# Kernel tuning notes

Measured on AMD Instinct MI355X. Metric: run time of the kernel, lower is better.

Reference implementation:

```python
import jax, jax.numpy as jnp
import numpy as np

V, D, NH, T_MAX, L, MLP = 50257, 1024, 16, 1024, 12, 4
HD = D // NH
F = D * MLP
B, T = 2, 1024


def setup_inputs() -> dict:
    key = jax.random.key(0)
    ks = jax.random.split(key, 16)
    s = 0.02
    inp = {
        'tokens': jax.random.randint(ks[0], (B, T), 0, V, dtype=jnp.int32),
        'wte': jax.random.normal(ks[1], (V, D), jnp.float32) * s,
        'wpe': jax.random.normal(ks[2], (T_MAX, D), jnp.float32) * s,
        'ln1_w': jnp.ones((L, D)), 'ln1_b': jnp.zeros((L, D)),
        'attn_w': jax.random.normal(ks[3], (L, D, 3 * D), jnp.float32) * s,
        'attn_b': jnp.zeros((L, 3 * D)),
        'aproj_w': jax.random.normal(ks[4], (L, D, D), jnp.float32) * s,
        'aproj_b': jnp.zeros((L, D)),
        'ln2_w': jnp.ones((L, D)), 'ln2_b': jnp.zeros((L, D)),
        'fc_w': jax.random.normal(ks[5], (L, D, F), jnp.float32) * s,
        'fc_b': jnp.zeros((L, F)),
        'proj_w': jax.random.normal(ks[6], (L, F, D), jnp.float32) * s,
        'proj_b': jnp.zeros((L, D)),
        'lnf_w': jnp.ones((D,)), 'lnf_b': jnp.zeros((D,)),
    }
    return inp


def _ln(x, w, b, eps=1e-5):
    m = jnp.mean(x, -1, keepdims=True)
    v = jnp.var(x, -1, keepdims=True)
    return (x - m) * jax.lax.rsqrt(v + eps) * w + b


def _forward(tokens, wte, wpe, ln1_w, ln1_b, attn_w, attn_b, aproj_w, aproj_b,
             ln2_w, ln2_b, fc_w, fc_b, proj_w, proj_b, lnf_w, lnf_b):
    b, t = tokens.shape
    x = wte[tokens] + wpe[:t]  # [B,T,D]
    scale = HD ** -0.5
    causal = jnp.tril(jnp.ones((t, t), bool))  # [T,T]

    def block(x, p):
        l1w, l1b, aw, ab, apw, apb, l2w, l2b, fw, fb, pw, pb = p
        h = _ln(x, l1w, l1b)
        qkv = h @ aw + ab  # [B,T,3D]
        q, k, v = jnp.split(qkv, 3, axis=-1)
        # rearrange 'b t (h n) -> b n t h' with n=NH: last dim is (head_size, n_heads)
        def split_heads(u):
            return u.reshape(b, t, HD, NH).transpose(0, 3, 1, 2)  # [B,NH,T,HD]
        q, k, v = split_heads(q), split_heads(k), split_heads(v)
        scores = jnp.einsum('bnth,bnsh->bnts', q, k) * scale
        scores = jnp.where(causal, scores, -jnp.inf)
        w = jax.nn.softmax(scores, axis=-1)
        att = jnp.einsum('bnts,bnsh->bnth', w, v)
        # rearrange 'b n t h -> b t (n h)'
        att = att.transpose(0, 2, 1, 3).reshape(b, t, D)
        x = x + (att @ apw + apb)
        h2 = _ln(x, l2w, l2b)
        x = x + (jax.nn.gelu(h2 @ fw + fb, approximate=False) @ pw + pb)
        return x, None

    params = (ln1_w, ln1_b, attn_w, attn_b, aproj_w, aproj_b,
              ln2_w, ln2_b, fc_w, fc_b, proj_w, proj_b)
    x, _ = jax.lax.scan(block, x, params)
    x = _ln(x, lnf_w, lnf_b)[:, -1:, :]  # [B,1,D]
    return x @ wte.T  # tied lm_head -> [B,1,V]


def reference(tokens, wte, wpe, ln1_w, ln1_b, attn_w, attn_b, aproj_w, aproj_b,
              ln2_w, ln2_b, fc_w, fc_b, proj_w, proj_b, lnf_w, lnf_b):
    return _forward(tokens, wte, wpe, ln1_w, ln1_b, attn_w, attn_b, aproj_w,
                    aproj_b, ln2_w, ln2_b, fc_w, fc_b, proj_w, proj_b, lnf_w, lnf_b)
```

## Files before the change

kernel.cpp:

```cpp
#include <hip/hip_runtime.h>
#include <cstdint>
#include <math.h>


using u16 = unsigned short;
using bf16x8 = __attribute__((ext_vector_type(8))) short;
using f32x4 = __attribute__((ext_vector_type(4))) float;

#define GLDS16(g, l)                                                        \
  __builtin_amdgcn_global_load_lds(                                         \
      (const __attribute__((address_space(1))) void*)(g),                   \
      (__attribute__((address_space(3))) void*)(l), 16, 0, 0)

__device__ __forceinline__ u16 f2bf(float f) {
  union { float f; unsigned u; } t; t.f = f;
  unsigned r = t.u + 0x7fffu + ((t.u >> 16) & 1u);
  return (u16)(r >> 16);
}

__device__ __forceinline__ float fast_erf(float x) {
  float ax = fabsf(x);
  float t = 1.f / (1.f + 0.3275911f * ax);
  float y = t * (0.254829592f +
            t * (-0.284496736f +
            t * (1.421413741f +
            t * (-1.453152027f +
            t * 1.061405429f))));
  float r = 1.f - y * __expf(-ax * ax);
  return copysignf(r, x);
}

#define DD 1024
#define TTT 1024
#define MR 2048
#define FFF 4096
#define VVV 50257

__global__ __launch_bounds__(256) void k_embed(const int* __restrict__ tokens,
                                               const float* __restrict__ wte,
                                               const float* __restrict__ wpe,
                                               float* __restrict__ x) {
  int m = blockIdx.x, d = threadIdx.x * 4;
  int t = m & (TTT - 1);
  int tok = tokens[m];
  const float4 a = *(const float4*)(wte + (size_t)tok * DD + d);
  const float4 p = *(const float4*)(wpe + (size_t)t * DD + d);
  float4 o; o.x = a.x + p.x; o.y = a.y + p.y; o.z = a.z + p.z; o.w = a.w + p.w;
  *(float4*)(x + (size_t)m * DD + d) = o;
}

__device__ __forceinline__ void addln_body(float* __restrict__ x,
                                           const float* __restrict__ pp, int npart,
                                           const float* __restrict__ w,
                                           const float* __restrict__ b,
                                           u16* __restrict__ out, int blk) {
  const int wid = threadIdx.x >> 6, lane = threadIdx.x & 63;
  const int m = blk * 4 + wid;
  float* row = x + (size_t)m * DD;
  float4 v[4];
  float s = 0.f, q = 0.f;
#pragma unroll
  for (int j = 0; j < 4; ++j) {
    v[j] = *(const float4*)(row + j * 256 + lane * 4);
    for (int p = 0; p < npart; ++p) {
      const float4 pv = *(const float4*)(pp + (size_t)p * MR * DD + (size_t)m * DD + j * 256 + lane * 4);
      v[j].x += pv.x; v[j].y += pv.y; v[j].z += pv.z; v[j].w += pv.w;
    }
    if (npart) *(float4*)(row + j * 256 + lane * 4) = v[j];
    s += v[j].x + v[j].y + v[j].z + v[j].w;
    q += v[j].x * v[j].x + v[j].y * v[j].y + v[j].z * v[j].z + v[j].w * v[j].w;
  }
#pragma unroll
  for (int off = 1; off < 64; off <<= 1) { s += __shfl_xor(s, off); q += __shfl_xor(q, off); }
  float mean = s * (1.f / DD);
  float var = q * (1.f / DD) - mean * mean;
  float rs = rsqrtf(var + 1e-5f);
#pragma unroll
  for (int j = 0; j < 4; ++j) {
    const float4 wv = *(const float4*)(w + j * 256 + lane * 4);
    const float4 bv = *(const float4*)(b + j * 256 + lane * 4);
    u16 o[4];
    o[0] = f2bf((v[j].x - mean) * rs * wv.x + bv.x);
    o[1] = f2bf((v[j].y - mean) * rs * wv.y + bv.y);
    o[2] = f2bf((v[j].z - mean) * rs * wv.z + bv.z);
    o[3] = f2bf((v[j].w - mean) * rs * wv.w + bv.w);
    *(uint64_t*)(out + (size_t)m * DD + j * 256 + lane * 4) = *(uint64_t*)o;
  }
}

__global__ __launch_bounds__(256) void k_addln(float* __restrict__ x,
                                               const float* __restrict__ pp, int npart,
                                               const float* __restrict__ w,
                                               const float* __restrict__ b,
                                               u16* __restrict__ out) {
  addln_body(x, pp, npart, w, b, out, blockIdx.x);
}

__device__ __forceinline__ void wtrans_body(const float* __restrict__ atw,
                                            const float* __restrict__ apw,
                                            const float* __restrict__ fcw,
                                            const float* __restrict__ pjw,
                                            u16* __restrict__ wt, int id) {
  __shared__ u16 tb[64][72];
  const float* W; u16* Wt; int K, N, local, kts;
  if (id < 768)       { W = atw; Wt = wt;           K = 1024; N = 3072; local = id;        kts = 4; }
  else if (id < 1024) { W = apw; Wt = wt + 3145728; K = 1024; N = 1024; local = id - 768;  kts = 4; }
  else if (id < 2048) { W = fcw; Wt = wt + 4194304; K = 1024; N = 4096; local = id - 1024; kts = 4; }
  else                { W = pjw; Wt = wt + 8388608; K = 4096; N = 1024; local = id - 2048; kts = 6; }
  const int k0 = (local & ((1 << kts) - 1)) * 64, n0 = (local >> kts) * 64;
  const int tid = threadIdx.x;
  const int rr = tid >> 4, c4 = (tid & 15) * 4;
#pragma unroll
  for (int i = 0; i < 4; ++i) {
    const int r = rr + i * 16;
    const float4 v = *(const float4*)(W + (size_t)(k0 + r) * N + n0 + c4);
    tb[c4 + 0][r] = f2bf(v.x);
    tb[c4 + 1][r] = f2bf(v.y);
    tb[c4 + 2][r] = f2bf(v.z);
    tb[c4 + 3][r] = f2bf(v.w);
  }
  __syncthreads();
  const int n = tid >> 3, k8 = (tid & 7) * 8;
#pragma unroll
  for (int s = 0; s < 2; ++s) {
    u16 o[8];
#pragma unroll
    for (int j = 0; j < 8; ++j) o[j] = tb[n + s * 32][k8 + j];
    *(bf16x8*)(Wt + (size_t)(n0 + n + s * 32) * K + k0 + k8) = *(bf16x8*)o;
  }
}

__global__ __launch_bounds__(256) void k_prep(float* __restrict__ x,
                                              const float* __restrict__ pp, int npart,
                                              const float* __restrict__ w,
                                              const float* __restrict__ b,
                                              u16* __restrict__ out,
                                              const float* __restrict__ atw,
                                              const float* __restrict__ apw,
                                              const float* __restrict__ fcw,
                                              const float* __restrict__ pjw,
                                              u16* __restrict__ wt) {
  if (blockIdx.x < 512) {
    addln_body(x, pp, npart, w, b, out, blockIdx.x);
  } else {
    wtrans_body(atw, apw, fcw, pjw, wt, blockIdx.x - 512);
  }
}

template <int EPI>
__global__ __launch_bounds__(256) void k_gemm(const u16* __restrict__ A,
                                              const u16* __restrict__ Bt,
                                              const float* __restrict__ bias,
                                              u16* __restrict__ outb,
                                              float* __restrict__ pp,
                                              int M, int N, int K, int KC) {
  __shared__ u16 As[2][128 * 64];
  __shared__ u16 Bs[2][128 * 64];
  const int nbx = gridDim.x, nby = gridDim.y;
  const int nwg = nbx * nby * gridDim.z;
  const int orig = blockIdx.x + nbx * (blockIdx.y + nby * blockIdx.z);
  const int qq = nwg >> 3, rr = nwg & 7;
  const int xcd = orig & 7, pos = orig >> 3;
  const int wg = (xcd < rr ? xcd * (qq + 1) : rr * (qq + 1) + (xcd - rr) * qq) + pos;
  const int bx = wg % nbx;
  const int tmpw = wg / nbx;
  const int by = tmpw % nby, bz = tmpw / nby;

  const int tid = threadIdx.x;
  const int lane = tid & 63, wid = tid >> 6;
  const int wr = wid >> 1, wc = wid & 1;
  const int l15 = lane & 15, l4 = lane >> 4;
  const int sx = l15 & 7;
  const int m0 = bx * 128, n0 = by * 128;
  f32x4 acc[4][4] = {};

  const int srow = tid >> 3;
  const int scol = (((tid & 7) ^ (srow & 7)) * 8);
  const int k0beg = bz * KC;
  const int nt = KC >> 6;

  const u16* Ap = A + (size_t)(m0 + srow) * K + scol;
  const u16* Bp = Bt + (size_t)(n0 + srow) * K + scol;

#define STAGE(buf, k0)                                                      \
  {                                                                         \
    _Pragma("unroll")                                                       \
    for (int it = 0; it < 4; ++it) {                                        \
      GLDS16(Ap + (size_t)it * 32 * K + (k0), (char*)As[buf] + it * 4096 + tid * 16); \
      GLDS16(Bp + (size_t)it * 32 * K + (k0), (char*)Bs[buf] + it * 4096 + tid * 16); \
    }                                                                       \
  }

  STAGE(0, k0beg);
  for (int t = 0; t < nt; ++t) {
    if (t + 1 < nt) {
      STAGE((t + 1) & 1, k0beg + (t + 1) * 64);
      asm volatile("s_waitcnt vmcnt(8)" ::: "memory");
    } else {
      asm volatile("s_waitcnt vmcnt(0)" ::: "memory");
    }
    __builtin_amdgcn_sched_barrier(0);
    __builtin_amdgcn_s_barrier();
    __builtin_amdgcn_sched_barrier(0);
    const u16* Ab = As[t & 1];
    const u16* Bb = Bs[t & 1];
#pragma unroll
    for (int ks = 0; ks < 2; ++ks) {
      const int ch = ((ks * 4 + l4) ^ sx) * 8;
      bf16x8 af[4], bfr[4];
#pragma unroll
      for (int i = 0; i < 4; ++i)
        af[i] = *(const bf16x8*)(Ab + (wr * 64 + i * 16 + l15) * 64 + ch);
#pragma unroll
      for (int j = 0; j < 4; ++j)
        bfr[j] = *(const bf16x8*)(Bb + (wc * 64 + j * 16 + l15) * 64 + ch);
      __builtin_amdgcn_s_setprio(1);
#pragma unroll
      for (int i = 0; i < 4; ++i)
#pragma unroll
        for (int j = 0; j < 4; ++j)
          acc[i][j] = __builtin_amdgcn_mfma_f32_16x16x32_bf16(af[i], bfr[j], acc[i][j], 0, 0, 0);
      __builtin_amdgcn_s_setprio(0);
    }
    __builtin_amdgcn_sched_barrier(0);
    __builtin_amdgcn_s_barrier();
    __builtin_amdgcn_sched_barrier(0);
  }
#undef STAGE
  float* ppz = (EPI == 4) ? pp + (size_t)bz * M * N : nullptr;
#pragma unroll
  for (int j = 0; j < 4; ++j) {
    const int col = n0 + wc * 64 + j * 16 + l15;
    const float bs = (EPI == 4 && bz != 0) ? 0.f : bias[col];
#pragma unroll
    for (int i = 0; i < 4; ++i) {
#pragma unroll
      for (int r = 0; r < 4; ++r) {
        const int row = m0 + wr * 64 + i * 16 + l4 * 4 + r;
        float v = acc[i][j][r] + bs;
        if (EPI == 0) {
          outb[(size_t)row * N + col] = f2bf(v);
        } else if (EPI == 2) {
          float g = 0.5f * v * (1.f + fast_erf(v * 0.70710678118f));
          outb[(size_t)row * N + col] = f2bf(g);
        } else {
          ppz[(size_t)row * N + col] = v;
        }
      }
    }
  }
}

__global__ __launch_bounds__(256) void k_repack(const u16* __restrict__ qkv,
                                                u16* __restrict__ Kb,
                                                u16* __restrict__ Vt) {
  __shared__ u16 tile[16 * 1024];
  const int tid = threadIdx.x;
  const int m0 = blockIdx.x * 16;
  const int part = blockIdx.y + 1;
  const int b = m0 >> 10;
  const int tg0 = m0 & (TTT - 1);
#pragma unroll
  for (int p = 0; p < 8; ++p) {
    int row = p * 2 + (tid >> 7);
    int col8 = (tid & 127) * 8;
    bf16x8 v = *(const bf16x8*)(qkv + (size_t)(m0 + row) * 3072 + part * 1024 + col8);
    int e = col8 ^ (((col8 >> 4) & 7) << 3);
    *(bf16x8*)(tile + row * 1024 + e) = v;
  }
  __syncthreads();
  const int lane = tid & 63, wid = tid >> 6;
  if (part == 1) {
    for (int p = wid; p < 256; p += 4) {
      int t = p >> 4, n = p & 15;
      int e = (lane * 16 + n) ^ ((lane & 7) << 3);
      u16 val = tile[t * 1024 + e];
      Kb[(((size_t)(b * 16 + n)) * TTT + tg0 + t) * 64 + lane] = val;
    }
  } else {
    for (int p = wid; p < 32; p += 4) {
      int n = p >> 1, tc = p & 1;
      int e = (lane * 16 + n) ^ ((lane & 7) << 3);
      u16 val8[8];
#pragma unroll
      for (int k = 0; k < 8; ++k) val8[k] = tile[(tc * 8 + k) * 1024 + e];
      *(bf16x8*)(Vt + (((size_t)(b * 16 + n)) * 64 + lane) * TTT + tg0 + tc * 8) =
          *(bf16x8*)val8;
    }
  }
}

__global__ __launch_bounds__(256) void k_attn(const u16* __restrict__ qkv,
                                              const u16* __restrict__ Kb,
                                              const u16* __restrict__ Vt,
                                              u16* __restrict__ attout) {
  __shared__ u16 Ks[128 * 64];
  __shared__ u16 Vs[64 * 128];
  __shared__ u16 Ps[4][16 * 136];

  const int tid = threadIdx.x;
  const int lane = tid & 63, wid = tid >> 6;
  const int l15 = lane & 15, l4 = lane >> 4;
  const int bn = blockIdx.x;
  const int b = bn >> 4, nh = bn & 15;
  const char* Kg0 = (const char*)(Kb + (size_t)bn * TTT * 64);
  const char* Vg0 = (const char*)(Vt + (size_t)bn * 64 * TTT);

#pragma unroll
  for (int pass = 0; pass < 2; ++pass) {
    const int qtr = pass == 0 ? 15 - (int)blockIdx.y : (int)blockIdx.y;
    const int q0 = qtr * 64;

    const int qrow = q0 + wid * 16 + l15;
    const u16* qsrc = qkv + (size_t)(b * TTT + qrow) * 3072 + nh;
    bf16x8 aq[2];
#pragma unroll
    for (int ks = 0; ks < 2; ++ks) {
      short tmp[8];
#pragma unroll
      for (int j = 0; j < 8; ++j) tmp[j] = (short)qsrc[(ks * 32 + l4 * 8 + j) * 16];
      aq[ks] = *(bf16x8*)tmp;
    }

    float m_run[4], l_part[4];
    f32x4 o[4] = {};
#pragma unroll
    for (int r = 0; r < 4; ++r) { m_run[r] = -1e30f; l_part[r] = 0.f; }

    const int ntk = (qtr >> 1) + 1;
    for (int kt = 0; kt < ntk; ++kt) {
#pragma unroll
      for (int it = 0; it < 4; ++it) {
        int L = it * 4096 + tid * 16;
        int Ls = L ^ (((L >> 7) & 7) << 4);
        GLDS16(Kg0 + (size_t)kt * 16384 + Ls, (char*)Ks + L);
      }
#pragma unroll
      for (int it = 0; it < 4; ++it) {
        int L = it * 4096 + tid * 16;
        int Ls = L ^ (((L >> 8) & 7) << 4);
        int hrow = Ls >> 8, cb = Ls & 255;
        GLDS16(Vg0 + (size_t)hrow * 2048 + kt * 256 + cb, (char*)Vs + L);
      }
      __syncthreads();

      f32x4 sf[8];
#pragma unroll
      for (int cf = 0; cf < 8; ++cf) {
        f32x4 z = {};
#pragma unroll
        for (int ks = 0; ks < 2; ++ks) {
          int P = (cf * 16 + l15) * 128 + (ks * 32 + l4 * 8) * 2;
          bf16x8 kb = *(const bf16x8*)((const char*)Ks + (P ^ (((P >> 7) & 7) << 4)));
          z = __builtin_amdgcn_mfma_f32_16x16x32_bf16(aq[ks], kb, z, 0, 0, 0);
        }
        sf[cf] = z;
      }
      const bool lastkt = (kt == ntk - 1);
#pragma unroll
      for (int cf = 0; cf < 8; ++cf)
#pragma unroll
        for (int r = 0; r < 4; ++r) {
          float s = sf[cf][r] * 0.125f;
          if (lastkt) {
            int kg = kt * 128 + cf * 16 + l15;
            int qg = q0 + wid * 16 + l4 * 4 + r;
            if (kg > qg) s = -1e30f;
          }
          sf[cf][r] = s;
        }
      float fac[4];
#pragma unroll
      for (int r = 0; r < 4; ++r) {
        float tm = sf[0][r];
#pragma unroll
        for (int cf = 1; cf < 8; ++cf) tm = fmaxf(tm, sf[cf][r]);
#pragma unroll
        for (int off = 1; off < 16; off <<= 1) tm = fmaxf(tm, __shfl_xor(tm, off));
        float mnew = fmaxf(m_run[r], tm);
        fac[r] = __expf(m_run[r] - mnew);
        m_run[r] = mnew;
        float ps = 0.f;
#pragma unroll
        for (int cf = 0; cf < 8; ++cf) {
          float p = __expf(sf[cf][r] - mnew);
          sf[cf][r] = p;
          ps += p;
        }
        l_part[r] = l_part[r] * fac[r] + ps;
      }
#pragma unroll
      for (int cf = 0; cf < 8; ++cf)
#pragma unroll
        for (int r = 0; r < 4; ++r)
          Ps[wid][(l4 * 4 + r) * 136 + cf * 16 + l15] = f2bf(sf[cf][r]);
#pragma unroll
      for (int hf = 0; hf < 4; ++hf)
#pragma unroll
        for (int r = 0; r < 4; ++r) o[hf][r] *= fac[r];
      bf16x8 pa[4];
#pragma unroll
      for (int ks = 0; ks < 4; ++ks)
        pa[ks] = *(const bf16x8*)&Ps[wid][l15 * 136 + ks * 32 + l4 * 8];
#pragma unroll
      for (int hf = 0; hf < 4; ++hf) {
#pragma unroll
        for (int ks = 0; ks < 4; ++ks) {
          int P = (hf * 16 + l15) * 256 + (ks * 32 + l4 * 8) * 2;
          bf16x8 vb = *(const bf16x8*)((const char*)Vs + (P ^ (((P >> 8) & 7) << 4)));
          o[hf] = __builtin_amdgcn_mfma_f32_16x16x32_bf16(pa[ks], vb, o[hf], 0, 0, 0);
        }
      }
      __syncthreads();
    }
    float lsum[4];
#pragma unroll
    for (int r = 0; r < 4; ++r) {
      float s = l_part[r];
#pragma unroll
      for (int off = 1; off < 16; off <<= 1) s += __shfl_xor(s, off);
      lsum[r] = s;
    }
#pragma unroll
    for (int hf = 0; hf < 4; ++hf)
#pragma unroll
      for (int r = 0; r < 4; ++r) {
        float val = o[hf][r] / lsum[r];
        size_t row = (size_t)b * TTT + q0 + wid * 16 + l4 * 4 + r;
        attout[row * DD + nh * 64 + hf * 16 + l15] = f2bf(val);
      }
  }
}

__global__ __launch_bounds__(256) void k_head(const float* __restrict__ x,
                                              const float* __restrict__ pp, int npart,
                                              const float* __restrict__ lnf_w,
                                              const float* __restrict__ lnf_b,
                                              const float* __restrict__ wte,
                                              float* __restrict__ out) {
  __shared__ float xs[2 * DD];
  __shared__ float sm[8];
  int tid = threadIdx.x;
  int wid = tid >> 6, lane = tid & 63;
#pragma unroll
  for (int bb = 0; bb < 2; ++bb) {
    int m = bb * TTT + (TTT - 1);
    float4 v = *(const float4*)(x + (size_t)m * DD + tid * 4);
    for (int p = 0; p < npart; ++p) {
      const float4 pv = *(const float4*)(pp + (size_t)p * MR * DD + (size_t)m * DD + tid * 4);
      v.x += pv.x; v.y += pv.y; v.z += pv.z; v.w += pv.w;
    }
    float s = v.x + v.y + v.z + v.w;
    float q = v.x * v.x + v.y * v.y + v.z * v.z + v.w * v.w;
#pragma unroll
    for (int off = 1; off < 64; off <<= 1) { s += __shfl_xor(s, off); q += __shfl_xor(q, off); }
    if ((tid & 63) == 0) { sm[wid] = s; sm[4 + wid] = q; }
    __syncthreads();
    s = sm[0] + sm[1] + sm[2] + sm[3];
    q = sm[4] + sm[5] + sm[6] + sm[7];
    float mean = s * (1.f / DD);
    float var = q * (1.f / DD) - mean * mean;
    float rs = rsqrtf(var + 1e-5f);
    const float4 wv = *(const float4*)(lnf_w + tid * 4);
    const float4 bv = *(const float4*)(lnf_b + tid * 4);
    float4 o;
    o.x = (v.x - mean) * rs * wv.x + bv.x;
    o.y = (v.y - mean) * rs * wv.y + bv.y;
    o.z = (v.z - mean) * rs * wv.z + bv.z;
    o.w = (v.w - mean) * rs * wv.w + bv.w;
    *(float4*)(xs + bb * DD + tid * 4) = o;
    __syncthreads();
  }
  for (int v = blockIdx.x * 4 + wid; v < VVV; v += gridDim.x * 4) {
    const float* wr = wte + (size_t)v * DD;
    float a0 = 0.f, a1 = 0.f;
#pragma unroll
    for (int j = 0; j < 4; ++j) {
      const float4 wv = *(const float4*)(wr + lane * 16 + j * 4);
      const float4 x0 = *(const float4*)(xs + lane * 16 + j * 4);
      const float4 x1 = *(const float4*)(xs + DD + lane * 16 + j * 4);
      a0 += wv.x * x0.x + wv.y * x0.y + wv.z * x0.z + wv.w * x0.w;
      a1 += wv.x * x1.x + wv.y * x1.y + wv.z * x1.z + wv.w * x1.w;
    }
#pragma unroll
    for (int off = 1; off < 64; off <<= 1) { a0 += __shfl_xor(a0, off); a1 += __shfl_xor(a1, off); }
    if (lane == 0) { out[v] = a0; out[VVV + v] = a1; }
  }
}

extern "C" void kernel_launch(void* const* d_in, const int* in_sizes, int n_in,
                              void* d_out, int out_size, void* d_ws, size_t ws_size,
                              hipStream_t stream) {
  const int* tokens    = (const int*)d_in[0];
  const float* wte     = (const float*)d_in[1];
  const float* wpe     = (const float*)d_in[2];
  const float* ln1_w   = (const float*)d_in[3];
  const float* ln1_b   = (const float*)d_in[4];
  const float* attn_w  = (const float*)d_in[5];
  const float* attn_b  = (const float*)d_in[6];
  const float* aproj_w = (const float*)d_in[7];
  const float* aproj_b = (const float*)d_in[8];
  const float* ln2_w   = (const float*)d_in[9];
  const float* ln2_b   = (const float*)d_in[10];
  const float* fc_w    = (const float*)d_in[11];
  const float* fc_b    = (const float*)d_in[12];
  const float* proj_w  = (const float*)d_in[13];
  const float* proj_b  = (const float*)d_in[14];
  const float* lnf_w   = (const float*)d_in[15];
  const float* lnf_b   = (const float*)d_in[16];

  char* ws = (char*)d_ws;
  float* x    = (float*)(ws);
  u16* h      = (u16*)(ws + (8u << 20));
  u16* wt     = (u16*)(ws + (12u << 20));
  u16* qkv    = (u16*)(ws + (36u << 20));
  u16* Kb     = (u16*)(ws + (48u << 20));
  u16* Vt     = (u16*)(ws + (52u << 20));
  u16* attb   = (u16*)(ws + (56u << 20));
  u16* mlph   = (u16*)(ws + (36u << 20));
  float* pp   = (float*)(ws + (60u << 20));
  float* out  = (float*)d_out;

  u16* atw = wt;
  u16* apw = wt + 3145728;
  u16* fcw = wt + 4194304;
  u16* pjw = wt + 8388608;

  k_embed<<<MR, 256, 0, stream>>>(tokens, wte, wpe, x);

  for (int l = 0; l < 12; ++l) {
    k_prep<<<3584, 256, 0, stream>>>(x, pp, l == 0 ? 0 : 4,
                                     ln1_w + l * DD, ln1_b + l * DD, h,
                                     attn_w + (size_t)l * DD * 3 * DD,
                                     aproj_w + (size_t)l * DD * DD,
                                     fc_w + (size_t)l * DD * FFF,
                                     proj_w + (size_t)l * FFF * DD, wt);
    k_gemm<0><<<dim3(16, 24, 1), 256, 0, stream>>>(h, atw, attn_b + (size_t)l * 3 * DD, qkv, nullptr, MR, 3072, 1024, 1024);
    k_repack<<<dim3(128, 2), 256, 0, stream>>>(qkv, Kb, Vt);
    k_attn<<<dim3(32, 8), 256, 0, stream>>>(qkv, Kb, Vt, attb);
    k_gemm<4><<<dim3(16, 8, 2), 256, 0, stream>>>(attb, apw, aproj_b + (size_t)l * DD, nullptr, pp, MR, 1024, 1024, 512);
    k_addln<<<512, 256, 0, stream>>>(x, pp, 2, ln2_w + l * DD, ln2_b + l * DD, h);
    k_gemm<2><<<dim3(16, 32, 1), 256, 0, stream>>>(h, fcw, fc_b + (size_t)l * FFF, mlph, nullptr, MR, 4096, 1024, 1024);
    k_gemm<4><<<dim3(16, 8, 4), 256, 0, stream>>>(mlph, pjw, proj_b + (size_t)l * DD, nullptr, pp, MR, 1024, 4096, 1024);
  }
  k_head<<<512, 256, 0, stream>>>(x, pp, 4, lnf_w, lnf_b, wte, out);
}
```

Before: 1.921 ms.

## Permute QKV weight columns to head-major order and drop K repack

The QKV weight transpose now reorders output columns so that each head's 64 dimensions are contiguous. A separate block permutes the bias to match. Attention then reads K directly from the qkv buffer with strided async loads, and Q with vector loads, so the K half of the repack kernel and its scalar global stores go away. The cost is an extra bias buffer, one extra block in the prep kernel, and K tile loads that now stride across qkv rows.

Measured after the change: 1.857 ms. 3.4% less time.

```diff
diff --git a/kernel.cpp b/kernel.cpp
--- a/kernel.cpp
+++ b/kernel.cpp
@@ -102,8 +102,8 @@
                                             const float* __restrict__ pjw,
                                             u16* __restrict__ wt, int id) {
   __shared__ u16 tb[64][72];
-  const float* W; u16* Wt; int K, N, local, kts;
-  if (id < 768)       { W = atw; Wt = wt;           K = 1024; N = 3072; local = id;        kts = 4; }
+  const float* W; u16* Wt; int K, N, local, kts; bool perm = false;
+  if (id < 768)       { W = atw; Wt = wt;           K = 1024; N = 3072; local = id;        kts = 4; perm = true; }
   else if (id < 1024) { W = apw; Wt = wt + 3145728; K = 1024; N = 1024; local = id - 768;  kts = 4; }
   else if (id < 2048) { W = fcw; Wt = wt + 4194304; K = 1024; N = 4096; local = id - 1024; kts = 4; }
   else                { W = pjw; Wt = wt + 8388608; K = 4096; N = 1024; local = id - 2048; kts = 6; }
@@ -126,7 +126,12 @@
     u16 o[8];
 #pragma unroll
     for (int j = 0; j < 8; ++j) o[j] = tb[n + s * 32][k8 + j];
-    *(bf16x8*)(Wt + (size_t)(n0 + n + s * 32) * K + k0 + k8) = *(bf16x8*)o;
+    int orow = n0 + n + s * 32;
+    if (perm) {
+      int part = orow >> 10, w = orow & 1023;
+      orow = part * 1024 + (w & 15) * 64 + (w >> 4);
+    }
+    *(bf16x8*)(Wt + (size_t)orow * K + k0 + k8) = *(bf16x8*)o;
   }
 }
 
@@ -139,9 +144,16 @@
                                               const float* __restrict__ apw,
                                               const float* __restrict__ fcw,
                                               const float* __restrict__ pjw,
-                                              u16* __restrict__ wt) {
+                                              u16* __restrict__ wt,
+                                              const float* __restrict__ ab,
+                                              float* __restrict__ pbias) {
   if (blockIdx.x < 512) {
     addln_body(x, pp, npart, w, b, out, blockIdx.x);
+  } else if (blockIdx.x == 3584) {
+    for (int c = threadIdx.x; c < 3072; c += 256) {
+      int part = c >> 10, ww = c & 1023;
+      pbias[c] = ab[part * 1024 + (ww & 63) * 16 + (ww >> 6)];
+    }
   } else {
     wtrans_body(atw, apw, fcw, pjw, wt, blockIdx.x - 512);
   }
@@ -252,46 +264,32 @@
 }
 
 __global__ __launch_bounds__(256) void k_repack(const u16* __restrict__ qkv,
-                                                u16* __restrict__ Kb,
                                                 u16* __restrict__ Vt) {
-  __shared__ u16 tile[16 * 1024];
+  __shared__ u16 tile[16][1032];
   const int tid = threadIdx.x;
   const int m0 = blockIdx.x * 16;
-  const int part = blockIdx.y + 1;
   const int b = m0 >> 10;
   const int tg0 = m0 & (TTT - 1);
 #pragma unroll
   for (int p = 0; p < 8; ++p) {
     int row = p * 2 + (tid >> 7);
     int col8 = (tid & 127) * 8;
-    bf16x8 v = *(const bf16x8*)(qkv + (size_t)(m0 + row) * 3072 + part * 1024 + col8);
-    int e = col8 ^ (((col8 >> 4) & 7) << 3);
-    *(bf16x8*)(tile + row * 1024 + e) = v;
+    bf16x8 v = *(const bf16x8*)(qkv + (size_t)(m0 + row) * 3072 + 2048 + col8);
+    *(bf16x8*)(&tile[row][col8]) = v;
   }
   __syncthreads();
   const int lane = tid & 63, wid = tid >> 6;
-  if (part == 1) {
-    for (int p = wid; p < 256; p += 4) {
-      int t = p >> 4, n = p & 15;
-      int e = (lane * 16 + n) ^ ((lane & 7) << 3);
-      u16 val = tile[t * 1024 + e];
-      Kb[(((size_t)(b * 16 + n)) * TTT + tg0 + t) * 64 + lane] = val;
-    }
-  } else {
-    for (int p = wid; p < 32; p += 4) {
-      int n = p >> 1, tc = p & 1;
-      int e = (lane * 16 + n) ^ ((lane & 7) << 3);
-      u16 val8[8];
-#pragma unroll
-      for (int k = 0; k < 8; ++k) val8[k] = tile[(tc * 8 + k) * 1024 + e];
-      *(bf16x8*)(Vt + (((size_t)(b * 16 + n)) * 64 + lane) * TTT + tg0 + tc * 8) =
-          *(bf16x8*)val8;
-    }
+  for (int p = wid; p < 32; p += 4) {
+    int n = p >> 1, tc = p & 1;
+    u16 o[8];
+#pragma unroll
+    for (int k = 0; k < 8; ++k) o[k] = tile[tc * 8 + k][n * 64 + lane];
+    *(bf16x8*)(Vt + (((size_t)(b * 16 + n)) * 64 + lane) * TTT + tg0 + tc * 8) =
+        *(bf16x8*)o;
   }
 }
 
 __global__ __launch_bounds__(256) void k_attn(const u16* __restrict__ qkv,
-                                              const u16* __restrict__ Kb,
                                               const u16* __restrict__ Vt,
                                               u16* __restrict__ attout) {
   __shared__ u16 Ks[128 * 64];
@@ -303,7 +301,7 @@
   const int l15 = lane & 15, l4 = lane >> 4;
   const int bn = blockIdx.x;
   const int b = bn >> 4, nh = bn & 15;
-  const char* Kg0 = (const char*)(Kb + (size_t)bn * TTT * 64);
+  const char* Kg0 = (const char*)(qkv + (size_t)b * TTT * 3072 + 1024 + nh * 64);
   const char* Vg0 = (const char*)(Vt + (size_t)bn * 64 * TTT);
 
 #pragma unroll
@@ -312,15 +310,11 @@
     const int q0 = qtr * 64;
 
     const int qrow = q0 + wid * 16 + l15;
-    const u16* qsrc = qkv + (size_t)(b * TTT + qrow) * 3072 + nh;
+    const u16* qsrc = qkv + (size_t)(b * TTT + qrow) * 3072 + nh * 64;
     bf16x8 aq[2];
 #pragma unroll
-    for (int ks = 0; ks < 2; ++ks) {
-      short tmp[8];
-#pragma unroll
-      for (int j = 0; j < 8; ++j) tmp[j] = (short)qsrc[(ks * 32 + l4 * 8 + j) * 16];
-      aq[ks] = *(bf16x8*)tmp;
-    }
+    for (int ks = 0; ks < 2; ++ks)
+      aq[ks] = *(const bf16x8*)(qsrc + ks * 32 + l4 * 8);
 
     float m_run[4], l_part[4];
     f32x4 o[4] = {};
@@ -333,7 +327,8 @@
       for (int it = 0; it < 4; ++it) {
         int L = it * 4096 + tid * 16;
         int Ls = L ^ (((L >> 7) & 7) << 4);
-        GLDS16(Kg0 + (size_t)kt * 16384 + Ls, (char*)Ks + L);
+        int krow = Ls >> 7, cb = Ls & 127;
+        GLDS16(Kg0 + (size_t)(kt * 128 + krow) * 6144 + cb, (char*)Ks + L);
       }
 #pragma unroll
       for (int it = 0; it < 4; ++it) {
@@ -514,11 +509,11 @@
   u16* h      = (u16*)(ws + (8u << 20));
   u16* wt     = (u16*)(ws + (12u << 20));
   u16* qkv    = (u16*)(ws + (36u << 20));
-  u16* Kb     = (u16*)(ws + (48u << 20));
   u16* Vt     = (u16*)(ws + (52u << 20));
   u16* attb   = (u16*)(ws + (56u << 20));
   u16* mlph   = (u16*)(ws + (36u << 20));
   float* pp   = (float*)(ws + (60u << 20));
+  float* pbias = (float*)(ws + (92u << 20));
   float* out  = (float*)d_out;
 
   u16* atw = wt;
@@ -529,15 +524,16 @@
   k_embed<<<MR, 256, 0, stream>>>(tokens, wte, wpe, x);
 
   for (int l = 0; l < 12; ++l) {
-    k_prep<<<3584, 256, 0, stream>>>(x, pp, l == 0 ? 0 : 4,
+    k_prep<<<3585, 256, 0, stream>>>(x, pp, l == 0 ? 0 : 4,
                                      ln1_w + l * DD, ln1_b + l * DD, h,
                                      attn_w + (size_t)l * DD * 3 * DD,
                                      aproj_w + (size_t)l * DD * DD,
                                      fc_w + (size_t)l * DD * FFF,
-                                     proj_w + (size_t)l * FFF * DD, wt);
-    k_gemm<0><<<dim3(16, 24, 1), 256, 0, stream>>>(h, atw, attn_b + (size_t)l * 3 * DD, qkv, nullptr, MR, 3072, 1024, 1024);
-    k_repack<<<dim3(128, 2), 256, 0, stream>>>(qkv, Kb, Vt);
-    k_attn<<<dim3(32, 8), 256, 0, stream>>>(qkv, Kb, Vt, attb);
+                                     proj_w + (size_t)l * FFF * DD, wt,
+                                     attn_b + (size_t)l * 3 * DD, pbias);
+    k_gemm<0><<<dim3(16, 24, 1), 256, 0, stream>>>(h, atw, pbias, qkv, nullptr, MR, 3072, 1024, 1024);
+    k_repack<<<128, 256, 0, stream>>>(qkv, Vt);
+    k_attn<<<dim3(32, 8), 256, 0, stream>>>(qkv, Vt, attb);
     k_gemm<4><<<dim3(16, 8, 2), 256, 0, stream>>>(attb, apw, aproj_b + (size_t)l * DD, nullptr, pp, MR, 1024, 1024, 512);
     k_addln<<<512, 256, 0, stream>>>(x, pp, 2, ln2_w + l * DD, ln2_b + l * DD, h);
     k_gemm<2><<<dim3(16, 32, 1), 256, 0, stream>>>(h, fcw, fc_b + (size_t)l * FFF, mlph, nullptr, MR, 4096, 1024, 1024);
```
